# Kernel tuning notes

Measured on AMD Instinct MI355X. Metric: run time of the kernel, lower is better.

The kernel has to match this reference:

```python
import jax, jax.numpy as jnp
import numpy as np
from jax import lax

B, H, W, Q = 2, 64, 64, 65536
HID, ENC = 256, 64


def _conv3x3(x, w, b):
    # x: (B,Cin,H,W), w: (Cout,Cin,3,3)
    y = lax.conv_general_dilated(x, w, (1, 1), ((1, 1), (1, 1)),
                                 dimension_numbers=("NCHW", "OIHW", "NCHW"))
    return y + b[None, :, None, None]


def _forward(inp, coord, cell, enc_w, enc_b, coef_w, coef_b, freq_w, freq_b,
             phase_w, w0, b0, w1, b1, w2, b2, w3, b3, wo, bo, gamma, beta):
    bs, q = coord.shape[:2]
    h, w = inp.shape[-2], inp.shape[-1]
    feat = _conv3x3(inp, enc_w, enc_b)          # (B,ENC,h,w)
    coef = _conv3x3(feat, coef_w, coef_b)       # (B,HID,h,w)
    freq = _conv3x3(feat, freq_w, freq_b)       # (B,HID,h,w)

    rx, ry = 1.0 / h, 1.0 / w                  # 2/h/2, 2/w/2
    eps_shift = 1e-6
    gather = jax.vmap(lambda f, y, x: f[:, y, x])  # (C,h,w),(q,),(q,) -> (C,q)

    mlp_ws = ((w0, b0), (w1, b1), (w2, b2), (w3, b3))
    rel_cell = cell * jnp.array([h, w], dtype=cell.dtype)  # (B,q,2)
    phase_term = jnp.einsum('bqc,kc->bqk', rel_cell, phase_w)  # (B,q,HID//2)

    preds, areas = [], []
    for vx in (-1, 1):
        for vy in (-1, 1):
            cy = jnp.clip(coord[..., 0] + vx * rx + eps_shift, -1 + 1e-6, 1 - 1e-6)
            cx = jnp.clip(coord[..., 1] + vy * ry + eps_shift, -1 + 1e-6, 1 - 1e-6)
            # nearest grid_sample, align_corners=False
            iy = jnp.clip(jnp.round((cy + 1) * h / 2 - 0.5), 0, h - 1).astype(jnp.int32)
            ix = jnp.clip(jnp.round((cx + 1) * w / 2 - 0.5), 0, w - 1).astype(jnp.int32)
            q_coef = gather(coef, iy, ix).transpose(0, 2, 1)   # (B,q,HID)
            q_freq = gather(freq, iy, ix).transpose(0, 2, 1)   # (B,q,HID)
            # nearest-sampled feat_coord == center coord of chosen pixel
            qy = -1.0 + (2.0 * iy.astype(coord.dtype) + 1.0) / h
            qx = -1.0 + (2.0 * ix.astype(coord.dtype) + 1.0) / w
            rel = jnp.stack([(coord[..., 0] - qy) * h,
                             (coord[..., 1] - qx) * w], axis=-1)  # (B,q,2)
            # split into pairs: qf[...,k,c] = q_freq[...,2k+c]
            qf = q_freq.reshape(bs, q, HID // 2, 2)
            qf = jnp.einsum('bqkc,bqc->bqk', qf, rel)            # (B,q,HID//2)
            qf = qf + phase_term
            fourier = jnp.concatenate([jnp.cos(np.pi * qf), jnp.sin(np.pi * qf)], axis=-1)
            x = (q_coef * fourier).reshape(bs * q, HID)
            hcur = x
            for wl, bl in mlp_ws:
                hcur = jax.nn.relu(hcur @ wl.T + bl)
            pred = (hcur @ wo.T + bo).reshape(bs, q, -1)         # (B,q,3)
            preds.append(pred)
            areas.append(jnp.abs(rel[..., 0] * rel[..., 1]) + 1e-9)

    tot_area = areas[0] + areas[1] + areas[2] + areas[3]
    # diagonal area swap: pred[i] weighted by areas[3-i]
    ret = sum(preds[i] * (areas[3 - i] / tot_area)[..., None] for i in range(4))

    # bilinear grid_sample residual, padding_mode='border', align_corners=False
    fy = (coord[..., 0] + 1) * h / 2 - 0.5
    fx = (coord[..., 1] + 1) * w / 2 - 0.5
    y0 = jnp.floor(fy); x0 = jnp.floor(fx)
    wy = (fy - y0)[:, None, :]; wx = (fx - x0)[:, None, :]       # (B,1,q)
    y0c = jnp.clip(y0, 0, h - 1).astype(jnp.int32)
    y1c = jnp.clip(y0 + 1, 0, h - 1).astype(jnp.int32)
    x0c = jnp.clip(x0, 0, w - 1).astype(jnp.int32)
    x1c = jnp.clip(x0 + 1, 0, w - 1).astype(jnp.int32)
    v00 = gather(inp, y0c, x0c); v01 = gather(inp, y0c, x1c)
    v10 = gather(inp, y1c, x0c); v11 = gather(inp, y1c, x1c)     # (B,3,q)
    res = (v00 * (1 - wy) * (1 - wx) + v01 * (1 - wy) * wx
           + v10 * wy * (1 - wx) + v11 * wy * wx)
    ret = ret + res.transpose(0, 2, 1)                           # (B,q,3)

    # BatchNorm1d(3) in training mode: per-channel stats over (batch, length)
    mean = ret.mean(axis=(0, 1))
    var = ret.var(axis=(0, 1))
    out = (ret - mean) * jax.lax.rsqrt(var + 1e-5) * gamma + beta
    return out


def setup_inputs() -> dict:
    key = jax.random.key(0)
    ks = jax.random.split(key, 16)

    def p(k, shape, fan):
        return jax.random.normal(k, shape, jnp.float32) * (1.0 / np.sqrt(fan))

    d = {}
    d['inp'] = jax.random.normal(ks[0], (B, 3, H, W), jnp.float32)
    d['coord'] = jax.random.uniform(ks[1], (B, Q, 2), jnp.float32, -1.0, 1.0)
    d['cell'] = jnp.full((B, Q, 2), 2.0 / 256.0, jnp.float32)
    d['enc_w'] = p(ks[2], (ENC, 3, 3, 3), 3 * 9)
    d['enc_b'] = jnp.zeros((ENC,), jnp.float32)
    d['coef_w'] = p(ks[3], (HID, ENC, 3, 3), ENC * 9)
    d['coef_b'] = jnp.zeros((HID,), jnp.float32)
    d['freq_w'] = p(ks[4], (HID, ENC, 3, 3), ENC * 9)
    d['freq_b'] = jnp.zeros((HID,), jnp.float32)
    d['phase_w'] = p(ks[5], (HID // 2, 2), 2)
    for i in range(4):
        d[f'w{i}'] = p(ks[6 + i], (HID, HID), HID)
        d[f'b{i}'] = jnp.zeros((HID,), jnp.float32)
    d['wo'] = p(ks[10], (3, HID), HID)
    d['bo'] = jnp.zeros((3,), jnp.float32)
    d['gamma'] = jnp.ones((3,), jnp.float32)
    d['beta'] = jnp.zeros((3,), jnp.float32)
    return d


def reference(inp, coord, cell, enc_w, enc_b, coef_w, coef_b, freq_w, freq_b,
              phase_w, w0, b0, w1, b1, w2, b2, w3, b3, wo, bo, gamma, beta):
    return _forward(inp, coord, cell, enc_w, enc_b, coef_w, coef_b, freq_w,
                    freq_b, phase_w, w0, b0, w1, b1, w2, b2, w3, b3, wo, bo,
                    gamma, beta)
```

## Files before the change

kernel.cpp:

```cpp
#include <hip/hip_runtime.h>

#define BQ   2
#define QQ   65536
#define HID  256
#define ENC  64
#define NPIX 4096
#define KCONV 576
#define NROW (BQ*QQ*4)

using bf16x8 = __bf16 __attribute__((ext_vector_type(8)));
using bf16x4 = __bf16 __attribute__((ext_vector_type(4)));
using f32x4  = float  __attribute__((ext_vector_type(4)));

__device__ __forceinline__ unsigned short f2bf(float f){
  unsigned u = __float_as_uint(f);
  u = (u + 0x7fffu + ((u >> 16) & 1u)) >> 16;
  return (unsigned short)u;
}
__device__ __forceinline__ float2 bf2x(unsigned u){
  float2 r;
  r.x = __uint_as_float(u << 16);
  r.y = __uint_as_float(u & 0xffff0000u);
  return r;
}

__device__ __forceinline__ float sin_rev(float r){
  float f, s;
  asm("v_fract_f32 %0, %1" : "=v"(f) : "v"(r));
  asm("v_sin_f32 %0, %1"   : "=v"(s) : "v"(f));
  return s;
}

__device__ __forceinline__ int xaddr(int row, int col){
  return row*512 + ((((col >> 3) ^ (row & 7)) << 4) | ((col & 7) << 1));
}

__global__ void prep_kernel(const float* coef_w, const float* freq_w,
                            const float* w0, const float* w1,
                            const float* w2, const float* w3,
                            const float* wo,
                            unsigned short* Wcat, unsigned short* Wmlp,
                            unsigned short* wo_pad){
  int idx = blockIdx.x*256 + threadIdx.x;
  if (idx < 512*KCONV){
    int n = idx / KCONV, k = idx % KCONV;
    int j = k >> 6, cin = k & 63;
    const float* src = (n < 256) ? coef_w : freq_w;
    Wcat[idx] = f2bf(src[(n & 255)*KCONV + cin*9 + j]);
    return;
  }
  int i2 = idx - 512*KCONV;
  if (i2 < 4*65536){
    const float* wl = (i2 < 65536) ? w0 : (i2 < 131072) ? w1
                     : (i2 < 196608) ? w2 : w3;
    Wmlp[i2] = f2bf(wl[i2 & 65535]);
    return;
  }
  int i3 = i2 - 4*65536;
  if (i3 < 16*256){
    int c = i3 >> 8, k = i3 & 255;
    wo_pad[i3] = (c < 3) ? f2bf(wo[c*256 + k]) : (unsigned short)0;
  }
}

__global__ __launch_bounds__(256)
void enc_conv_kernel(const float* inp, const float* enc_w, const float* enc_b,
                     unsigned short* fpad){
  __shared__ float wl[ENC*27];
  __shared__ float bl2[ENC];
  int t = threadIdx.x;
  for (int i = t; i < ENC*27; i += 256) wl[i] = enc_w[i];
  if (t < ENC) bl2[t] = enc_b[t];
  __syncthreads();
  int px  = blockIdx.x*32 + (t >> 3);
  int oc0 = (t & 7)*8;
  int b = px >> 12, yx = px & 4095;
  int y = yx >> 6, x = yx & 63;
  float v[27];
  #pragma unroll
  for (int c = 0; c < 3; c++)
    #pragma unroll
    for (int dy = 0; dy < 3; dy++)
      #pragma unroll
      for (int dx = 0; dx < 3; dx++){
        int yy = y + dy - 1, xx = x + dx - 1;
        v[c*9 + dy*3 + dx] = (yy >= 0 && yy < 64 && xx >= 0 && xx < 64)
                             ? inp[(b*3 + c)*NPIX + yy*64 + xx] : 0.f;
      }
  bf16x8 o;
  #pragma unroll
  for (int oc = 0; oc < 8; oc++){
    float acc = bl2[oc0 + oc];
    #pragma unroll
    for (int k = 0; k < 27; k++) acc += wl[(oc0 + oc)*27 + k]*v[k];
    o[oc] = (__bf16)acc;
  }
  *(bf16x8*)(fpad + ((b*66 + y + 1)*66 + x + 1)*64 + oc0) = o;
}

__global__ __launch_bounds__(256)
void conv_gemm_kernel(const unsigned short* fpad, const unsigned short* Wcat,
                      const float* coef_b, const float* freq_b,
                      unsigned short* coefB, unsigned short* freqB){
  int wave = threadIdx.x >> 6, lane = threadIdx.x & 63;
  int l16 = lane & 15, g = lane >> 4;
  int tile = blockIdx.x*4 + wave;
  int nt = tile & 31, pt = tile >> 5;
  int gp = pt*16 + l16;
  int b = gp >> 12, y = (gp >> 6) & 63, x = gp & 63;
  const unsigned short* fbase = fpad + ((b*66 + y)*66 + x)*64;
  const unsigned short* Wp = Wcat + (nt*16 + l16)*KCONV + g*8;
  f32x4 acc;
  {
    const float* bsrc = (nt < 16) ? coef_b : freq_b;
    float4 b4 = *(const float4*)(bsrc + ((nt*16) & 255) + g*4);
    acc[0] = b4.x; acc[1] = b4.y; acc[2] = b4.z; acc[3] = b4.w;
  }
  #pragma unroll
  for (int kk = 0; kk < 18; kk++){
    int j = kk >> 1, dy = j/3, dx = j%3;
    bf16x8 bfrag = *(const bf16x8*)(fbase + (dy*66 + dx)*64 + (kk & 1)*32 + g*8);
    bf16x8 afrag = *(const bf16x8*)(Wp + kk*32);
    acc = __builtin_amdgcn_mfma_f32_16x16x32_bf16(afrag, bfrag, acc, 0, 0, 0);
  }
  bf16x4 o4;
  o4[0] = (__bf16)acc[0]; o4[1] = (__bf16)acc[1];
  o4[2] = (__bf16)acc[2]; o4[3] = (__bf16)acc[3];
  if (nt < 16) *(bf16x4*)(coefB + gp*256 + nt*16 + g*4)        = o4;
  else         *(bf16x4*)(freqB + gp*256 + (nt - 16)*16 + g*4) = o4;
}

__global__ __launch_bounds__(512, 4)
void mlp_kernel(const unsigned short* coefB, const unsigned short* freqB,
                const float* coord, const float* cell, const float* phase_w,
                const unsigned short* Wmlp,
                const float* b0, const float* b1, const float* b2, const float* b3,
                const unsigned short* wo_pad, const float* bo,
                float* areas, float* pred){
  __shared__ __align__(16) char Xs[128*256*2];
  __shared__ __align__(16) float geo[8][16][8];
  int t = threadIdx.x;
  int r0 = blockIdx.x*128;
  int wave = t >> 6, lane = t & 63;
  int l16 = lane & 15, g = lane >> 4;
  int lr0 = wave*16;

  if (lane < 16){
    int gr = r0 + lr0 + lane;
    int bq = gr >> 2, s = gr & 3;
    float2 crd = *(const float2*)(coord + bq*2);
    float2 cel = *(const float2*)(cell + bq*2);
    float vx = (s & 2) ? 1.f : -1.f;
    float vy = (s & 1) ? 1.f : -1.f;
    const float RX = 1.f/64.f;
    float cy = fminf(fmaxf(crd.x + vx*RX + 1e-6f, -1.f + 1e-6f), 1.f - 1e-6f);
    float cx = fminf(fmaxf(crd.y + vy*RX + 1e-6f, -1.f + 1e-6f), 1.f - 1e-6f);
    int iy = min(max((int)rintf((cy + 1.f)*32.f - 0.5f), 0), 63);
    int ix = min(max((int)rintf((cx + 1.f)*32.f - 0.5f), 0), 63);
    float qy = -1.f + (2*iy + 1)*RX;
    float qx = -1.f + (2*ix + 1)*RX;
    float rel0 = (crd.x - qy)*64.f;
    float rel1 = (crd.y - qx)*64.f;
    areas[gr] = fabsf(rel0*rel1) + 1e-9f;
    int b = gr >> 18;
    int pix = b*NPIX + iy*64 + ix;
    geo[wave][lane][0] = __int_as_float(pix);
    geo[wave][lane][1] = rel0;
    geo[wave][lane][2] = rel1;
    geo[wave][lane][3] = cel.x*64.f;
    geo[wave][lane][4] = cel.y*64.f;
  }
  float4 pw[4];
  #pragma unroll
  for (int j = 0; j < 4; j++)
    pw[j] = *(const float4*)(phase_w + 16*l16 + 4*j);
  __syncthreads();

  #pragma unroll
  for (int it = 0; it < 4; it++){
    int ri = it*4 + g;
    int lr = lr0 + ri;
    float4 g4 = *(const float4*)(&geo[wave][ri][0]);
    float ce1 = geo[wave][ri][4];
    int pix = __float_as_int(g4.x);
    float rel0 = g4.y, rel1 = g4.z, ce0 = g4.w;
    const unsigned short* fR = freqB + pix*256 + 16*l16;
    const unsigned short* cR = coefB + pix*256 + 8*l16;
    uint4 fva = *(const uint4*)(fR);
    uint4 fvb = *(const uint4*)(fR + 8);
    uint4 cca = *(const uint4*)(cR);
    uint4 csa = *(const uint4*)(cR + 128);
    bf16x8 cv, sv;
    #pragma unroll
    for (int j = 0; j < 4; j++){
      unsigned uf0 = (j==0)?fva.x:(j==1)?fva.z:(j==2)?fvb.x:fvb.z;
      unsigned uf1 = (j==0)?fva.y:(j==1)?fva.w:(j==2)?fvb.y:fvb.w;
      unsigned uc  = (j==0)?cca.x:(j==1)?cca.y:(j==2)?cca.z:cca.w;
      unsigned us  = (j==0)?csa.x:(j==1)?csa.y:(j==2)?csa.z:csa.w;
      float2 f01 = bf2x(uf0);
      float2 f23 = bf2x(uf1);
      float2 cab = bf2x(uc);
      float2 sab = bf2x(us);
      float4 pj = pw[j];
      float q0 = f01.x*rel0 + f01.y*rel1 + ce0*pj.x + ce1*pj.y;
      float q1 = f23.x*rel0 + f23.y*rel1 + ce0*pj.z + ce1*pj.w;
      cv[2*j]   = (__bf16)(sin_rev(q0*0.5f + 0.25f) * cab.x);
      sv[2*j]   = (__bf16)(sin_rev(q0*0.5f)         * sab.x);
      cv[2*j+1] = (__bf16)(sin_rev(q1*0.5f + 0.25f) * cab.y);
      sv[2*j+1] = (__bf16)(sin_rev(q1*0.5f)         * sab.y);
    }
    *(bf16x8*)(Xs + xaddr(lr, 8*l16))       = cv;
    *(bf16x8*)(Xs + xaddr(lr, 128 + 8*l16)) = sv;
  }

  int n0 = wave*32;
  bf16x8 wf0c = *(const bf16x8*)(Wmlp + (n0 + l16)*256      + g*8);
  bf16x8 wf1c = *(const bf16x8*)(Wmlp + (n0 + 16 + l16)*256 + g*8);
  __syncthreads();

  const float* const bls[4] = {b0, b1, b2, b3};

  #pragma unroll
  for (int l = 0; l < 4; l++){
    const unsigned short* Wl = Wmlp + l*65536;
    const unsigned short* Wn = Wmlp + (l < 3 ? (l+1)*65536 : l*65536);
    f32x4 acc[8][2];
    #pragma unroll
    for (int nt = 0; nt < 2; nt++){
      float4 bv = *(const float4*)(bls[l] + n0 + nt*16 + g*4);
      #pragma unroll
      for (int rt = 0; rt < 8; rt++){
        acc[rt][nt][0] = bv.x; acc[rt][nt][1] = bv.y;
        acc[rt][nt][2] = bv.z; acc[rt][nt][3] = bv.w;
      }
    }
    #pragma unroll
    for (int kk = 0; kk < 8; kk++){
      bf16x8 wf0n, wf1n;
      if (kk < 7){
        wf0n = *(const bf16x8*)(Wl + (n0 + l16)*256      + (kk+1)*32 + g*8);
        wf1n = *(const bf16x8*)(Wl + (n0 + 16 + l16)*256 + (kk+1)*32 + g*8);
      } else {
        wf0n = *(const bf16x8*)(Wn + (n0 + l16)*256      + g*8);
        wf1n = *(const bf16x8*)(Wn + (n0 + 16 + l16)*256 + g*8);
      }
      #pragma unroll
      for (int rt = 0; rt < 8; rt++){
        bf16x8 xf = *(const bf16x8*)(Xs + xaddr(rt*16 + l16, kk*32 + g*8));
        acc[rt][0] = __builtin_amdgcn_mfma_f32_16x16x32_bf16(wf0c, xf, acc[rt][0], 0,0,0);
        acc[rt][1] = __builtin_amdgcn_mfma_f32_16x16x32_bf16(wf1c, xf, acc[rt][1], 0,0,0);
      }
      wf0c = wf0n; wf1c = wf1n;
    }
    __syncthreads();
    #pragma unroll
    for (int rt = 0; rt < 8; rt++)
      #pragma unroll
      for (int nt = 0; nt < 2; nt++){
        int row = rt*16 + l16;
        int col = n0 + nt*16 + g*4;
        bf16x4 u;
        u[0] = (__bf16)fmaxf(acc[rt][nt][0], 0.f);
        u[1] = (__bf16)fmaxf(acc[rt][nt][1], 0.f);
        u[2] = (__bf16)fmaxf(acc[rt][nt][2], 0.f);
        u[3] = (__bf16)fmaxf(acc[rt][nt][3], 0.f);
        *(bf16x4*)(Xs + xaddr(row, col)) = u;
      }
    __syncthreads();
  }

  {
    f32x4 acc = {0.f, 0.f, 0.f, 0.f};
    #pragma unroll
    for (int kk = 0; kk < 8; kk++){
      bf16x8 wf = *(const bf16x8*)(wo_pad + l16*256 + kk*32 + g*8);
      bf16x8 xf = *(const bf16x8*)(Xs + xaddr(wave*16 + l16, kk*32 + g*8));
      acc = __builtin_amdgcn_mfma_f32_16x16x32_bf16(wf, xf, acc, 0, 0, 0);
    }
    if (g == 0){
      int row = r0 + wave*16 + l16;
      pred[row*3 + 0] = acc[0] + bo[0];
      pred[row*3 + 1] = acc[1] + bo[1];
      pred[row*3 + 2] = acc[2] + bo[2];
    }
  }
}

__global__ void combine_kernel(const float* pred, const float* areas,
                               const float* coord, const float* inp,
                               float* retbuf, float* partials){
  __shared__ float psum[8];
  int tid = threadIdx.x;
  if (tid < 8) psum[tid] = 0.f;
  __syncthreads();

  int bq = blockIdx.x*256 + tid;
  int b  = bq >> 16;
  float4 ar = *(const float4*)(areas + bq*4);
  float tot = ar.x + ar.y + ar.z + ar.w;
  float w0_ = ar.w/tot, w1_ = ar.z/tot, w2_ = ar.y/tot, w3_ = ar.x/tot;
  const float* pp = pred + bq*12;
  float r_[3];
  #pragma unroll
  for (int c = 0; c < 3; c++)
    r_[c] = pp[c]*w0_ + pp[3+c]*w1_ + pp[6+c]*w2_ + pp[9+c]*w3_;

  float c0 = coord[bq*2], c1 = coord[bq*2+1];
  float fy = (c0 + 1.f)*32.f - 0.5f, fx = (c1 + 1.f)*32.f - 0.5f;
  float y0f = floorf(fy), x0f = floorf(fx);
  float wy = fy - y0f, wx = fx - x0f;
  int y0 = min(max((int)y0f, 0), 63), y1 = min(max((int)y0f + 1, 0), 63);
  int x0 = min(max((int)x0f, 0), 63), x1 = min(max((int)x0f + 1, 0), 63);
  const float* ib = inp + b*3*NPIX;
  #pragma unroll
  for (int c = 0; c < 3; c++){
    const float* pl = ib + c*NPIX;
    float v00 = pl[y0*64 + x0], v01 = pl[y0*64 + x1];
    float v10 = pl[y1*64 + x0], v11 = pl[y1*64 + x1];
    r_[c] += v00*(1.f-wy)*(1.f-wx) + v01*(1.f-wy)*wx
           + v10*wy*(1.f-wx)       + v11*wy*wx;
    retbuf[bq*3 + c] = r_[c];
  }
  #pragma unroll
  for (int c = 0; c < 3; c++){
    float s = r_[c], ss = r_[c]*r_[c];
    #pragma unroll
    for (int off = 32; off; off >>= 1){
      s  += __shfl_down(s,  off);
      ss += __shfl_down(ss, off);
    }
    if ((tid & 63) == 0){
      atomicAdd(&psum[c],     s);
      atomicAdd(&psum[4 + c], ss);
    }
  }
  __syncthreads();
  if (tid < 8) partials[blockIdx.x*8 + tid] = psum[tid];
}

__global__ void reduce_kernel(const float* partials, float* bnsums){
  int t = threadIdx.x;
  int c = t >> 6;
  int i = t & 63;
  float s = 0.f;
  #pragma unroll
  for (int j = 0; j < 8; j++) s += partials[(i + 64*j)*8 + c];
  #pragma unroll
  for (int off = 32; off; off >>= 1) s += __shfl_down(s, off);
  if (i == 0) bnsums[c] = s;
}

__global__ void normalize_kernel(const float* retbuf, const float* bnsums,
                                 const float* gamma, const float* beta,
                                 float* out){
  int idx = blockIdx.x*256 + threadIdx.x;
  if (idx >= BQ*QQ*3) return;
  int c = idx % 3;
  const float n = (float)(BQ*QQ);
  float mean = bnsums[c] / n;
  float var  = bnsums[4 + c] / n - mean*mean;
  out[idx] = (retbuf[idx] - mean) * rsqrtf(var + 1e-5f) * gamma[c] + beta[c];
}

extern "C" void kernel_launch(void* const* d_in, const int* in_sizes, int n_in,
                              void* d_out, int out_size, void* d_ws, size_t ws_size,
                              hipStream_t stream){
  const float* inp    = (const float*)d_in[0];
  const float* coord  = (const float*)d_in[1];
  const float* cell   = (const float*)d_in[2];
  const float* enc_w  = (const float*)d_in[3];
  const float* enc_b  = (const float*)d_in[4];
  const float* coef_w = (const float*)d_in[5];
  const float* coef_b = (const float*)d_in[6];
  const float* freq_w = (const float*)d_in[7];
  const float* freq_b = (const float*)d_in[8];
  const float* phase_w= (const float*)d_in[9];
  const float* w0 = (const float*)d_in[10]; const float* b0 = (const float*)d_in[11];
  const float* w1 = (const float*)d_in[12]; const float* b1 = (const float*)d_in[13];
  const float* w2 = (const float*)d_in[14]; const float* b2 = (const float*)d_in[15];
  const float* w3 = (const float*)d_in[16]; const float* b3 = (const float*)d_in[17];
  const float* wo = (const float*)d_in[18]; const float* bo = (const float*)d_in[19];
  const float* gamma = (const float*)d_in[20]; const float* beta = (const float*)d_in[21];

  char* ws = (char*)d_ws;
  unsigned short* fpad   = (unsigned short*)(ws + 0);
  unsigned short* coefB  = (unsigned short*)(ws + 1116160);
  unsigned short* freqB  = (unsigned short*)(ws + 5310464);
  unsigned short* Wcat   = (unsigned short*)(ws + 9504768);
  unsigned short* Wmlp   = (unsigned short*)(ws + 10094592);
  unsigned short* wo_pad = (unsigned short*)(ws + 10618880);
  float*          areas  = (float*)(ws + 10627072);
  float*          pred   = (float*)(ws + 12724224);
  float*          retbuf = (float*)(ws + 19015680);
  float*          partials=(float*)(ws + 20588544);
  float*          bnsums = (float*)(ws + 20604928);
  if (ws_size < 20604960) return;

  hipMemsetAsync(fpad, 0, 1115136, stream);
  prep_kernel<<<2192, 256, 0, stream>>>(coef_w, freq_w, w0, w1, w2, w3, wo,
                                        Wcat, Wmlp, wo_pad);
  enc_conv_kernel<<<256, 256, 0, stream>>>(inp, enc_w, enc_b, fpad);
  conv_gemm_kernel<<<4096, 256, 0, stream>>>(fpad, Wcat, coef_b, freq_b,
                                             coefB, freqB);
  mlp_kernel<<<4096, 512, 0, stream>>>(coefB, freqB, coord, cell, phase_w, Wmlp,
                                       b0, b1, b2, b3, wo_pad, bo, areas, pred);
  combine_kernel<<<512, 256, 0, stream>>>(pred, areas, coord, inp, retbuf,
                                          partials);
  reduce_kernel<<<1, 512, 0, stream>>>(partials, bnsums);
  normalize_kernel<<<1536, 256, 0, stream>>>(retbuf, bnsums, gamma, beta,
                                             (float*)d_out);
}
```

Baseline: 408.8 us.

## Switch MLP kernel to 32x32x16 MFMA tiles with 64-row blocks

Measured after the change: 654.3 us. +60.1%, slower.

```diff
diff --git a/kernel.cpp b/kernel.cpp
--- a/kernel.cpp
+++ b/kernel.cpp
@@ -11,6 +11,7 @@
 using bf16x8 = __bf16 __attribute__((ext_vector_type(8)));
 using bf16x4 = __bf16 __attribute__((ext_vector_type(4)));
 using f32x4  = float  __attribute__((ext_vector_type(4)));
+using f32x16 = float  __attribute__((ext_vector_type(16)));
 
 __device__ __forceinline__ unsigned short f2bf(float f){
   unsigned u = __float_as_uint(f);
@@ -130,17 +131,17 @@
   else         *(bf16x4*)(freqB + gp*256 + (nt - 16)*16 + g*4) = o4;
 }
 
-__global__ __launch_bounds__(512, 4)
+__global__ __launch_bounds__(256, 4)
 void mlp_kernel(const unsigned short* coefB, const unsigned short* freqB,
                 const float* coord, const float* cell, const float* phase_w,
                 const unsigned short* Wmlp,
                 const float* b0, const float* b1, const float* b2, const float* b3,
                 const unsigned short* wo_pad, const float* bo,
                 float* areas, float* pred){
-  __shared__ __align__(16) char Xs[128*256*2];
-  __shared__ __align__(16) float geo[8][16][8];
+  __shared__ __align__(16) char Xs[64*256*2];
+  __shared__ __align__(16) float geo[4][16][8];
   int t = threadIdx.x;
-  int r0 = blockIdx.x*128;
+  int r0 = blockIdx.x*64;
   int wave = t >> 6, lane = t & 63;
   int l16 = lane & 15, g = lane >> 4;
   int lr0 = wave*16;
@@ -213,9 +214,10 @@
     *(bf16x8*)(Xs + xaddr(lr, 128 + 8*l16)) = sv;
   }
 
-  int n0 = wave*32;
-  bf16x8 wf0c = *(const bf16x8*)(Wmlp + (n0 + l16)*256      + g*8);
-  bf16x8 wf1c = *(const bf16x8*)(Wmlp + (n0 + 16 + l16)*256 + g*8);
+  int l32 = lane & 31, h = lane >> 5;
+  int n0 = wave*64;
+  bf16x8 wc0 = *(const bf16x8*)(Wmlp + (n0 +      l32)*256 + h*8);
+  bf16x8 wc1 = *(const bf16x8*)(Wmlp + (n0 + 32 + l32)*256 + h*8);
   __syncthreads();
 
   const float* const bls[4] = {b0, b1, b2, b3};
@@ -224,48 +226,57 @@
   for (int l = 0; l < 4; l++){
     const unsigned short* Wl = Wmlp + l*65536;
     const unsigned short* Wn = Wmlp + (l < 3 ? (l+1)*65536 : l*65536);
-    f32x4 acc[8][2];
-    #pragma unroll
-    for (int nt = 0; nt < 2; nt++){
-      float4 bv = *(const float4*)(bls[l] + n0 + nt*16 + g*4);
+    f32x16 acc0A, acc0B, acc1A, acc1B;
+    #pragma unroll
+    for (int nt = 0; nt < 2; nt++)
       #pragma unroll
-      for (int rt = 0; rt < 8; rt++){
-        acc[rt][nt][0] = bv.x; acc[rt][nt][1] = bv.y;
-        acc[rt][nt][2] = bv.z; acc[rt][nt][3] = bv.w;
+      for (int rg = 0; rg < 4; rg++){
+        float4 bv = *(const float4*)(bls[l] + n0 + nt*32 + rg*8 + h*4);
+        #pragma unroll
+        for (int j = 0; j < 4; j++){
+          if (nt == 0){ acc0A[rg*4+j] = ((const float*)&bv)[j];
+                        acc1A[rg*4+j] = ((const float*)&bv)[j]; }
+          else        { acc0B[rg*4+j] = ((const float*)&bv)[j];
+                        acc1B[rg*4+j] = ((const float*)&bv)[j]; }
+        }
       }
-    }
-    #pragma unroll
-    for (int kk = 0; kk < 8; kk++){
-      bf16x8 wf0n, wf1n;
-      if (kk < 7){
-        wf0n = *(const bf16x8*)(Wl + (n0 + l16)*256      + (kk+1)*32 + g*8);
-        wf1n = *(const bf16x8*)(Wl + (n0 + 16 + l16)*256 + (kk+1)*32 + g*8);
+    #pragma unroll
+    for (int kk = 0; kk < 16; kk++){
+      bf16x8 wn0, wn1;
+      if (kk < 15){
+        wn0 = *(const bf16x8*)(Wl + (n0 +      l32)*256 + (kk+1)*16 + h*8);
+        wn1 = *(const bf16x8*)(Wl + (n0 + 32 + l32)*256 + (kk+1)*16 + h*8);
       } else {
-        wf0n = *(const bf16x8*)(Wn + (n0 + l16)*256      + g*8);
-        wf1n = *(const bf16x8*)(Wn + (n0 + 16 + l16)*256 + g*8);
+        wn0 = *(const bf16x8*)(Wn + (n0 +      l32)*256 + h*8);
+        wn1 = *(const bf16x8*)(Wn + (n0 + 32 + l32)*256 + h*8);
       }
+      bf16x8 xf0 = *(const bf16x8*)(Xs + xaddr(     l32, kk*16 + h*8));
+      bf16x8 xf1 = *(const bf16x8*)(Xs + xaddr(32 + l32, kk*16 + h*8));
+      acc0A = __builtin_amdgcn_mfma_f32_32x32x16_bf16(wc0, xf0, acc0A, 0,0,0);
+      acc0B = __builtin_amdgcn_mfma_f32_32x32x16_bf16(wc1, xf0, acc0B, 0,0,0);
+      acc1A = __builtin_amdgcn_mfma_f32_32x32x16_bf16(wc0, xf1, acc1A, 0,0,0);
+      acc1B = __builtin_amdgcn_mfma_f32_32x32x16_bf16(wc1, xf1, acc1B, 0,0,0);
+      wc0 = wn0; wc1 = wn1;
+    }
+    __syncthreads();
+    #pragma unroll
+    for (int qt = 0; qt < 2; qt++){
+      int row = qt*32 + l32;
       #pragma unroll
-      for (int rt = 0; rt < 8; rt++){
-        bf16x8 xf = *(const bf16x8*)(Xs + xaddr(rt*16 + l16, kk*32 + g*8));
-        acc[rt][0] = __builtin_amdgcn_mfma_f32_16x16x32_bf16(wf0c, xf, acc[rt][0], 0,0,0);
-        acc[rt][1] = __builtin_amdgcn_mfma_f32_16x16x32_bf16(wf1c, xf, acc[rt][1], 0,0,0);
-      }
-      wf0c = wf0n; wf1c = wf1n;
-    }
-    __syncthreads();
-    #pragma unroll
-    for (int rt = 0; rt < 8; rt++)
-      #pragma unroll
-      for (int nt = 0; nt < 2; nt++){
-        int row = rt*16 + l16;
-        int col = n0 + nt*16 + g*4;
-        bf16x4 u;
-        u[0] = (__bf16)fmaxf(acc[rt][nt][0], 0.f);
-        u[1] = (__bf16)fmaxf(acc[rt][nt][1], 0.f);
-        u[2] = (__bf16)fmaxf(acc[rt][nt][2], 0.f);
-        u[3] = (__bf16)fmaxf(acc[rt][nt][3], 0.f);
-        *(bf16x4*)(Xs + xaddr(row, col)) = u;
-      }
+      for (int nt = 0; nt < 2; nt++)
+        #pragma unroll
+        for (int rg = 0; rg < 4; rg++){
+          const f32x16& a = (qt==0) ? (nt==0 ? acc0A : acc0B)
+                                    : (nt==0 ? acc1A : acc1B);
+          int coln = n0 + nt*32 + rg*8 + h*4;
+          bf16x4 u;
+          u[0] = (__bf16)fmaxf(a[rg*4+0], 0.f);
+          u[1] = (__bf16)fmaxf(a[rg*4+1], 0.f);
+          u[2] = (__bf16)fmaxf(a[rg*4+2], 0.f);
+          u[3] = (__bf16)fmaxf(a[rg*4+3], 0.f);
+          *(bf16x4*)(Xs + xaddr(row, coln)) = u;
+        }
+    }
     __syncthreads();
   }
 
@@ -402,7 +413,7 @@
   enc_conv_kernel<<<256, 256, 0, stream>>>(inp, enc_w, enc_b, fpad);
   conv_gemm_kernel<<<4096, 256, 0, stream>>>(fpad, Wcat, coef_b, freq_b,
                                              coefB, freqB);
-  mlp_kernel<<<4096, 512, 0, stream>>>(coefB, freqB, coord, cell, phase_w, Wmlp,
+  mlp_kernel<<<8192, 256, 0, stream>>>(coefB, freqB, coord, cell, phase_w, Wmlp,
                                        b0, b1, b2, b3, wo_pad, bo, areas, pred);
   combine_kernel<<<512, 256, 0, stream>>>(pred, areas, coord, inp, retbuf,
                                           partials);
```
